# Kernel tuning notes

Hardware: AMD Instinct MI355X
Metric: run time of the kernel (lower is better)

The kernel has to match this reference:

```python
import jax, jax.numpy as jnp
import numpy as np

N_CLUSTERS = 2048
EMBED_DIM = 512
DECAY = 0.99
EPSILON = 1e-05
NORM_EPS = 1e-12  # torch F.normalize default eps


def setup_inputs() -> dict:
    key = jax.random.key(0)
    k1, k2, k3, k4 = jax.random.split(key, 4)
    N = 32768
    return {
        "X": jax.random.normal(k1, (N, EMBED_DIM), dtype=jnp.float32),
        "centroids": jax.random.normal(k2, (N_CLUSTERS, EMBED_DIM), dtype=jnp.float32),
        "ema_cluster_size": jax.random.uniform(k3, (N_CLUSTERS,), dtype=jnp.float32),
        "ema_w": jax.random.normal(k4, (N_CLUSTERS, EMBED_DIM), dtype=jnp.float32),
    }


def reference(X, centroids, ema_cluster_size, ema_w):
    # --- distances on L2-normalized X (F.normalize(X, p=2, dim=1)) ---
    Xn = X / jnp.maximum(jnp.linalg.norm(X, axis=1, keepdims=True), NORM_EPS)
    distances = (
        jnp.sum(Xn * Xn, axis=1, keepdims=True)
        + jnp.sum(centroids * centroids, axis=1)
        - 2.0 * (Xn @ centroids.T)
    )
    cluster_indices = jnp.argmin(distances, axis=1)  # [N]
    onehot = jax.nn.one_hot(cluster_indices, N_CLUSTERS, dtype=X.dtype)  # [N,K]

    # quantized = onehot @ centroids  (gather form, same math)
    quantized = centroids[cluster_indices]  # [N,D]

    # --- EMA codebook update (uses ORIGINAL X, not normalized, per source) ---
    new_size = ema_cluster_size * DECAY + (1.0 - DECAY) * jnp.sum(onehot, axis=0)
    n = jnp.sum(new_size)
    new_size = (new_size + EPSILON) / (n + N_CLUSTERS * EPSILON) * n
    dw = onehot.T @ X  # [K,D] scatter-sum of assigned points
    new_w = ema_w * DECAY + (1.0 - DECAY) * dw
    new_centroids = new_w / new_size[:, None]

    return quantized, cluster_indices[:, None], new_centroids, new_size, new_w
```

## Files before the change

kernel.cpp:

```cpp
#include <hip/hip_runtime.h>
#include <hip/hip_bf16.h>
#include <stdint.h>

#define N_PTS    32768
#define N_CLU    2048
#define DIM      512
#define DECAY    0.99f
#define EPS      1e-5f
#define NORM_EPS 1e-12f
#define MARGIN   0.02f
#define WCAP     24576

#define OUT_Q      0
#define OUT_IDX    (N_PTS*DIM)
#define OUT_NEWC   (OUT_IDX + N_PTS)
#define OUT_SIZE   (OUT_NEWC + N_CLU*DIM)
#define OUT_NEWW   (OUT_SIZE + N_CLU)

typedef _Float16 half8 __attribute__((ext_vector_type(8)));
typedef float f32x4 __attribute__((ext_vector_type(4)));

union H8 { _Float16 h[8]; uint4 u; };

__device__ __forceinline__ unsigned enc_f32(float f) {
    unsigned u = __float_as_uint(f);
    return (u & 0x80000000u) ? ~u : (u | 0x80000000u);
}
__device__ __forceinline__ float dec_f32(unsigned e) {
    unsigned u = (e & 0x80000000u) ? (e & 0x7FFFFFFFu) : ~e;
    return __uint_as_float(u);
}

__global__ void init_kernel(int* __restrict__ counts,
                            int* __restrict__ cursor,
                            int* __restrict__ wl_cnt,
                            float* __restrict__ dw,
                            unsigned long long* __restrict__ best64) {
    int i = blockIdx.x * blockDim.x + threadIdx.x;
    int stride = gridDim.x * blockDim.x;
    if (i == 0) wl_cnt[0] = 0;
    for (int j = i; j < N_CLU; j += stride) { counts[j] = 0; cursor[j] = 0; }
    for (int j = i; j < N_CLU * DIM; j += stride) dw[j] = 0.0f;
    for (int j = i; j < WCAP; j += stride) best64[j] = 0xFFFFFFFFFFFFFFFFULL;
}

__global__ void prep_x_kernel(const float* __restrict__ X,
                              float* __restrict__ rnorm,
                              _Float16* __restrict__ Xh) {
    int row = (blockIdx.x * blockDim.x + threadIdx.x) >> 6;
    int lane = threadIdx.x & 63;
    if (row >= N_PTS) return;
    const float4* xr = (const float4*)(X + (size_t)row * DIM);
    float4 a = xr[2 * lane];
    float4 b = xr[2 * lane + 1];
    float ss = a.x*a.x + a.y*a.y + a.z*a.z + a.w*a.w
             + b.x*b.x + b.y*b.y + b.z*b.z + b.w*b.w;
    #pragma unroll
    for (int off = 32; off > 0; off >>= 1) ss += __shfl_xor(ss, off);
    float rs = 1.0f / fmaxf(sqrtf(ss), NORM_EPS);
    if (lane == 0) rnorm[row] = rs;
    H8 o;
    o.h[0] = (_Float16)(a.x * rs); o.h[1] = (_Float16)(a.y * rs);
    o.h[2] = (_Float16)(a.z * rs); o.h[3] = (_Float16)(a.w * rs);
    o.h[4] = (_Float16)(b.x * rs); o.h[5] = (_Float16)(b.y * rs);
    o.h[6] = (_Float16)(b.z * rs); o.h[7] = (_Float16)(b.w * rs);
    *(uint4*)(Xh + (size_t)row * DIM + lane * 8) = o.u;
}

__global__ void prep_c_kernel(const float* __restrict__ C,
                              float* __restrict__ cnorm2,
                              _Float16* __restrict__ Ch) {
    int row = (blockIdx.x * blockDim.x + threadIdx.x) >> 6;
    int lane = threadIdx.x & 63;
    if (row >= N_CLU) return;
    const float4* cr = (const float4*)(C + (size_t)row * DIM);
    float4 a = cr[2 * lane];
    float4 b = cr[2 * lane + 1];
    float ss = a.x*a.x + a.y*a.y + a.z*a.z + a.w*a.w
             + b.x*b.x + b.y*b.y + b.z*b.z + b.w*b.w;
    #pragma unroll
    for (int off = 32; off > 0; off >>= 1) ss += __shfl_xor(ss, off);
    if (lane == 0) cnorm2[row] = ss;
    H8 o;
    o.h[0] = (_Float16)a.x; o.h[1] = (_Float16)a.y;
    o.h[2] = (_Float16)a.z; o.h[3] = (_Float16)a.w;
    o.h[4] = (_Float16)b.x; o.h[5] = (_Float16)b.y;
    o.h[6] = (_Float16)b.z; o.h[7] = (_Float16)b.w;
    *(uint4*)(Ch + (size_t)row * DIM + lane * 8) = o.u;
}

#define TBM 128
#define TBN 128
#define TBK 32
#define LDS_S 40

__global__ __launch_bounds__(256) void dist_mfma_kernel(
    const _Float16* __restrict__ Xh, const _Float16* __restrict__ Ch,
    const float* __restrict__ cnorm2,
    unsigned long long* __restrict__ tile2) {
    __shared__ _Float16 Ah[TBM * LDS_S];
    __shared__ _Float16 Bh[TBN * LDS_S];

    const int tid = threadIdx.x;
    const int m0 = blockIdx.x * TBM;
    const int n0 = blockIdx.y * TBN;

    const int wid = tid >> 6;
    const int l = tid & 63;
    const int wr = wid >> 1, wc = wid & 1;
    const int lr = l & 15, g = l >> 4;

    const int srow = tid >> 1, shalf = tid & 1;
    const _Float16* srcA = Xh + (size_t)(m0 + srow) * DIM + shalf * 16;
    const _Float16* srcB = Ch + (size_t)(n0 + srow) * DIM + shalf * 16;
    _Float16* dstA = &Ah[srow * LDS_S + shalf * 16];
    _Float16* dstB = &Bh[srow * LDS_S + shalf * 16];

    f32x4 acc[4][4];
    #pragma unroll
    for (int m = 0; m < 4; m++)
        #pragma unroll
        for (int n = 0; n < 4; n++) acc[m][n] = (f32x4){0.f, 0.f, 0.f, 0.f};

    for (int k0 = 0; k0 < DIM; k0 += TBK) {
        const uint4* pa = (const uint4*)(srcA + k0);
        const uint4* pb = (const uint4*)(srcB + k0);
        uint4 a0 = pa[0], a1 = pa[1];
        uint4 b0 = pb[0], b1 = pb[1];
        *(uint4*)dstA = a0; *(uint4*)(dstA + 8) = a1;
        *(uint4*)dstB = b0; *(uint4*)(dstB + 8) = b1;
        __syncthreads();

        half8 af[4], bf[4];
        #pragma unroll
        for (int m = 0; m < 4; m++)
            af[m] = *(const half8*)&Ah[(wr * 64 + m * 16 + lr) * LDS_S + g * 8];
        #pragma unroll
        for (int n = 0; n < 4; n++)
            bf[n] = *(const half8*)&Bh[(wc * 64 + n * 16 + lr) * LDS_S + g * 8];
        #pragma unroll
        for (int m = 0; m < 4; m++)
            #pragma unroll
            for (int n = 0; n < 4; n++)
                acc[m][n] = __builtin_amdgcn_mfma_f32_16x16x32_f16(af[m], bf[n], acc[m][n], 0, 0, 0);
        __syncthreads();
    }

    float cn2[4];
    int coln[4];
    #pragma unroll
    for (int n = 0; n < 4; n++) {
        coln[n] = n0 + wc * 64 + n * 16 + lr;
        cn2[n] = cnorm2[coln[n]];
    }
    const int slot = blockIdx.y * 2 + wc;
    #pragma unroll
    for (int m = 0; m < 4; m++) {
        #pragma unroll
        for (int reg = 0; reg < 4; reg++) {
            unsigned long long b1 = ~0ULL, b2 = ~0ULL;
            #pragma unroll
            for (int n = 0; n < 4; n++) {
                float s = cn2[n] - 2.0f * acc[m][n][reg];
                unsigned long long p =
                    ((unsigned long long)enc_f32(s) << 32) | (unsigned)coln[n];
                if (p < b1) { b2 = b1; b1 = p; }
                else if (p < b2) { b2 = p; }
            }
            #pragma unroll
            for (int off = 1; off < 16; off <<= 1) {
                unsigned long long c1 = __shfl_xor(b1, off);
                unsigned long long c2 = __shfl_xor(b2, off);
                if (c1 < b1) { b2 = (b1 < c2) ? b1 : c2; b1 = c1; }
                else         { b2 = (b2 < c1) ? b2 : c1; }
            }
            if (lr == 0) {
                int R = m0 + wr * 64 + m * 16 + g * 4 + reg;
                size_t o = ((size_t)slot * N_PTS + R) * 2;
                tile2[o] = b1;
                tile2[o + 1] = b2;
            }
        }
    }
}

__global__ void reduce_kernel(const unsigned long long* __restrict__ tile2,
                              int* __restrict__ idxs,
                              int* __restrict__ wl, int* __restrict__ wl_cnt) {
    int i = blockIdx.x * blockDim.x + threadIdx.x;
    if (i >= N_PTS) return;
    unsigned long long b1 = ~0ULL, b2 = ~0ULL;
    #pragma unroll
    for (int j = 0; j < 32; j++) {
        size_t o = ((size_t)j * N_PTS + i) * 2;
        unsigned long long c1 = tile2[o], c2 = tile2[o + 1];
        if (c1 < b1) { b2 = (b1 < c2) ? b1 : c2; b1 = c1; }
        else         { b2 = (b2 < c1) ? b2 : c1; }
    }
    idxs[i] = (int)(unsigned)(b1 & 0xFFFFFFFFu);
    float gap = dec_f32((unsigned)(b2 >> 32)) - dec_f32((unsigned)(b1 >> 32));
    if (gap < MARGIN) {
        int pos = atomicAdd(wl_cnt, 1);
        wl[pos] = i;
    }
}

__global__ void gather_kernel(const float* __restrict__ X,
                              const float* __restrict__ rnorm,
                              const int* __restrict__ wl,
                              const int* __restrict__ wl_cnt,
                              float* __restrict__ Xg) {
    int gw = (blockIdx.x * blockDim.x + threadIdx.x) >> 6;
    int lane = threadIdx.x & 63;
    int n = wl_cnt[0];
    if (n > WCAP) n = WCAP;
    for (int pos = gw; pos < n; pos += 2048) {
        int i = wl[pos];
        float rs = rnorm[i];
        const float4* src = (const float4*)(X + (size_t)i * DIM);
        float4* dst = (float4*)(Xg + (size_t)pos * DIM);
        float4 a = src[2 * lane], b = src[2 * lane + 1];
        a.x *= rs; a.y *= rs; a.z *= rs; a.w *= rs;
        b.x *= rs; b.y *= rs; b.z *= rs; b.w *= rs;
        dst[2 * lane] = a;
        dst[2 * lane + 1] = b;
    }
}

#define BM 128
#define BN 128
#define BK 16

__global__ __launch_bounds__(256) void exact_tile_kernel(
    const float* __restrict__ Xg, const float* __restrict__ C,
    const float* __restrict__ cnorm2, const int* __restrict__ wl_cnt,
    unsigned long long* __restrict__ best64) {
    const int m0 = blockIdx.x * BM;
    int n = wl_cnt[0];
    if (n > WCAP) n = WCAP;
    if (m0 >= n) return;

    __shared__ float As[BK][BM];
    __shared__ float Bs[BK][BN];

    const int tid = threadIdx.x;
    const int tx = tid & 15;
    const int ty = tid >> 4;
    const int n0 = blockIdx.y * BN;

    const int f0 = tid;
    const int f1 = tid + 256;
    const int rowA0 = f0 >> 2, kq0 = f0 & 3;
    const int rowA1 = f1 >> 2, kq1 = f1 & 3;
    const float* Abase0 = Xg + (size_t)(m0 + rowA0) * DIM + kq0 * 4;
    const float* Abase1 = Xg + (size_t)(m0 + rowA1) * DIM + kq1 * 4;
    const float* Bbase0 = C + (size_t)(n0 + rowA0) * DIM + kq0 * 4;
    const float* Bbase1 = C + (size_t)(n0 + rowA1) * DIM + kq1 * 4;

    float acc[8][8];
    #pragma unroll
    for (int r = 0; r < 8; r++)
        #pragma unroll
        for (int c = 0; c < 8; c++) acc[r][c] = 0.0f;

    for (int c0 = 0; c0 < DIM; c0 += BK) {
        float4 va0 = *(const float4*)(Abase0 + c0);
        float4 va1 = *(const float4*)(Abase1 + c0);
        float4 vb0 = *(const float4*)(Bbase0 + c0);
        float4 vb1 = *(const float4*)(Bbase1 + c0);
        As[kq0*4+0][rowA0] = va0.x; As[kq0*4+1][rowA0] = va0.y;
        As[kq0*4+2][rowA0] = va0.z; As[kq0*4+3][rowA0] = va0.w;
        As[kq1*4+0][rowA1] = va1.x; As[kq1*4+1][rowA1] = va1.y;
        As[kq1*4+2][rowA1] = va1.z; As[kq1*4+3][rowA1] = va1.w;
        Bs[kq0*4+0][rowA0] = vb0.x; Bs[kq0*4+1][rowA0] = vb0.y;
        Bs[kq0*4+2][rowA0] = vb0.z; Bs[kq0*4+3][rowA0] = vb0.w;
        Bs[kq1*4+0][rowA1] = vb1.x; Bs[kq1*4+1][rowA1] = vb1.y;
        Bs[kq1*4+2][rowA1] = vb1.z; Bs[kq1*4+3][rowA1] = vb1.w;
        __syncthreads();

        #pragma unroll
        for (int t = 0; t < BK; t++) {
            float4 a0 = *(const float4*)&As[t][ty * 8];
            float4 a1 = *(const float4*)&As[t][ty * 8 + 4];
            float4 b0 = *(const float4*)&Bs[t][tx * 8];
            float4 b1 = *(const float4*)&Bs[t][tx * 8 + 4];
            float a[8] = {a0.x, a0.y, a0.z, a0.w, a1.x, a1.y, a1.z, a1.w};
            float b[8] = {b0.x, b0.y, b0.z, b0.w, b1.x, b1.y, b1.z, b1.w};
            #pragma unroll
            for (int r = 0; r < 8; r++)
                #pragma unroll
                for (int c = 0; c < 8; c++)
                    acc[r][c] = fmaf(a[r], b[c], acc[r][c]);
        }
        __syncthreads();
    }

    #pragma unroll
    for (int r = 0; r < 8; r++) {
        float bs = INFINITY;
        int bi = 0x7FFFFFFF;
        #pragma unroll
        for (int c = 0; c < 8; c++) {
            int gc = n0 + tx * 8 + c;
            float s = cnorm2[gc] - 2.0f * acc[r][c];
            if (s < bs) { bs = s; bi = gc; }
        }
        unsigned long long p =
            ((unsigned long long)enc_f32(bs) << 32) | (unsigned)bi;
        #pragma unroll
        for (int off = 1; off < 16; off <<= 1) {
            unsigned long long q = __shfl_xor(p, off);
            if (q < p) p = q;
        }
        if (tx == 0) atomicMin(best64 + m0 + ty * 8 + r, p);
    }
}

__global__ void writeback_kernel(const unsigned long long* __restrict__ best64,
                                 const int* __restrict__ wl,
                                 const int* __restrict__ wl_cnt,
                                 int* __restrict__ idxs) {
    int pos = blockIdx.x * blockDim.x + threadIdx.x;
    int n = wl_cnt[0];
    if (n > WCAP) n = WCAP;
    if (pos >= n) return;
    idxs[wl[pos]] = (int)(unsigned)(best64[pos] & 0xFFFFFFFFu);
}

__global__ __launch_bounds__(256) void exact_serial_kernel(
    const float* __restrict__ X, const float* __restrict__ C,
    const float* __restrict__ rnorm, const float* __restrict__ cnorm2,
    const int* __restrict__ wl, const int* __restrict__ wl_cnt,
    int* __restrict__ idxs) {
    int gw = (blockIdx.x * blockDim.x + threadIdx.x) >> 6;
    int lane = threadIdx.x & 63;
    int n = wl_cnt[0];
    for (int it = WCAP + gw; it < n; it += 1024) {
        int i = wl[it];
        float rs = rnorm[i];
        const float4* xr = (const float4*)(X + (size_t)i * DIM);
        float4 xa = xr[2 * lane], xb = xr[2 * lane + 1];
        xa.x *= rs; xa.y *= rs; xa.z *= rs; xa.w *= rs;
        xb.x *= rs; xb.y *= rs; xb.z *= rs; xb.w *= rs;
        unsigned long long best = ~0ULL;
        for (int k = 0; k < N_CLU; k++) {
            const float4* cr = (const float4*)(C + (size_t)k * DIM);
            float4 ca = cr[2 * lane], cb = cr[2 * lane + 1];
            float d = xa.x*ca.x + xa.y*ca.y + xa.z*ca.z + xa.w*ca.w
                    + xb.x*cb.x + xb.y*cb.y + xb.z*cb.z + xb.w*cb.w;
            #pragma unroll
            for (int off = 32; off > 0; off >>= 1) d += __shfl_xor(d, off);
            float s = cnorm2[k] - 2.0f * d;
            unsigned long long p =
                ((unsigned long long)enc_f32(s) << 32) | (unsigned)k;
            if (p < best) best = p;
        }
        if (lane == 0) idxs[i] = (int)(unsigned)(best & 0xFFFFFFFFu);
    }
}

__global__ void decode_kernel(const int* __restrict__ idxs,
                              float* __restrict__ out_idx,
                              int* __restrict__ counts) {
    int i = blockIdx.x * blockDim.x + threadIdx.x;
    if (i >= N_PTS) return;
    int lane = threadIdx.x & 63;
    int idx = idxs[i];
    out_idx[i] = (float)idx;
    unsigned long long remaining = __ballot(1);
    while (remaining) {
        int leader = __ffsll((unsigned long long)remaining) - 1;
        int k0 = __shfl(idx, leader);
        unsigned long long mask = __ballot(idx == k0);
        if (lane == leader) atomicAdd(&counts[k0], (int)__popcll(mask));
        remaining &= ~mask;
    }
}

__global__ void quant_kernel(const float* __restrict__ C,
                             const int* __restrict__ idxs,
                             float* __restrict__ outq) {
    int wave = (blockIdx.x * blockDim.x + threadIdx.x) >> 6;
    int lane = threadIdx.x & 63;
    if (wave >= N_PTS) return;
    int idx = idxs[wave];
    const float4* src = (const float4*)(C + (size_t)idx * DIM);
    float4* dst = (float4*)(outq + (size_t)wave * DIM);
    dst[lane] = src[lane];
    dst[lane + 64] = src[lane + 64];
}

__global__ __launch_bounds__(1024) void scan_kernel(const int* __restrict__ counts,
                                                    int* __restrict__ offsets) {
    __shared__ int bufA[N_CLU];
    __shared__ int bufB[N_CLU];
    int t = threadIdx.x;
    bufA[t] = counts[t];
    bufA[t + 1024] = counts[t + 1024];
    __syncthreads();
    int* src = bufA;
    int* dst = bufB;
    for (int d = 1; d < N_CLU; d <<= 1) {
        for (int i = t; i < N_CLU; i += 1024) {
            int v = src[i];
            if (i >= d) v += src[i - d];
            dst[i] = v;
        }
        __syncthreads();
        int* tmp = src; src = dst; dst = tmp;
    }
    for (int i = t; i < N_CLU; i += 1024)
        offsets[i] = (i == 0) ? 0 : src[i - 1];
}

__global__ void place_kernel(const int* __restrict__ idxs,
                             const int* __restrict__ offsets,
                             int* __restrict__ cursor,
                             int* __restrict__ bucket,
                             int* __restrict__ bkey) {
    int i = blockIdx.x * blockDim.x + threadIdx.x;
    if (i >= N_PTS) return;
    int lane = threadIdx.x & 63;
    int k = idxs[i];
    int pos = 0;
    unsigned long long remaining = __ballot(1);
    while (remaining) {
        int leader = __ffsll((unsigned long long)remaining) - 1;
        int k0 = __shfl(k, leader);
        unsigned long long mask = __ballot(k == k0);
        int base = 0;
        if (lane == leader) base = atomicAdd(&cursor[k0], (int)__popcll(mask));
        base = __shfl(base, leader);
        if (k == k0)
            pos = offsets[k0] + base +
                  (int)__popcll(mask & ((1ULL << lane) - 1ULL));
        remaining &= ~mask;
    }
    bucket[pos] = i;
    bkey[pos] = k;
}

__global__ __launch_bounds__(1024) void newsize_kernel(
    const float* __restrict__ ema_size, const int* __restrict__ counts,
    float* __restrict__ out_size) {
    __shared__ float red[16];
    __shared__ float nval;
    int t = threadIdx.x;
    float p0 = ema_size[t] * DECAY + (1.0f - DECAY) * (float)counts[t];
    float p1 = ema_size[t + 1024] * DECAY + (1.0f - DECAY) * (float)counts[t + 1024];
    float s = p0 + p1;
    #pragma unroll
    for (int off = 32; off > 0; off >>= 1) s += __shfl_xor(s, off);
    if ((t & 63) == 0) red[t >> 6] = s;
    __syncthreads();
    if (t == 0) {
        float n = 0.0f;
        for (int i = 0; i < 16; i++) n += red[i];
        nval = n;
    }
    __syncthreads();
    float n = nval;
    float denom = n + (float)N_CLU * EPS;
    out_size[t]        = (p0 + EPS) / denom * n;
    out_size[t + 1024] = (p1 + EPS) / denom * n;
}

#define CHUNK 64
__global__ __launch_bounds__(256) void dw_kernel(
    const float* __restrict__ X, const int* __restrict__ bucket,
    const int* __restrict__ bkey, float* __restrict__ dw) {
    int c0 = blockIdx.x * CHUNK;
    int t = threadIdx.x;
    float accx = 0.0f, accy = 0.0f;
    int prevk = bkey[c0];
    for (int j = 0; j < CHUNK; j++) {
        int pos = c0 + j;
        int k = bkey[pos];
        if (k != prevk) {
            atomicAdd(&dw[(size_t)prevk * DIM + t * 2 + 0], accx);
            atomicAdd(&dw[(size_t)prevk * DIM + t * 2 + 1], accy);
            accx = 0.0f; accy = 0.0f;
            prevk = k;
        }
        int p = bucket[pos];
        float2 v = *(const float2*)(X + (size_t)p * DIM + t * 2);
        accx += v.x; accy += v.y;
    }
    atomicAdd(&dw[(size_t)prevk * DIM + t * 2 + 0], accx);
    atomicAdd(&dw[(size_t)prevk * DIM + t * 2 + 1], accy);
}

__global__ void final_kernel(const float* __restrict__ ema_w,
                             const float* __restrict__ dw,
                             const float* __restrict__ new_size,
                             float* __restrict__ out_neww,
                             float* __restrict__ out_newc) {
    int e = blockIdx.x * blockDim.x + threadIdx.x;
    if (e >= N_CLU * DIM) return;
    int k = e >> 9;
    float nw = ema_w[e] * DECAY + (1.0f - DECAY) * dw[e];
    out_neww[e] = nw;
    out_newc[e] = nw / new_size[k];
}

extern "C" void kernel_launch(void* const* d_in, const int* in_sizes, int n_in,
                              void* d_out, int out_size, void* d_ws, size_t ws_size,
                              hipStream_t stream) {
    const float* X        = (const float*)d_in[0];
    const float* C        = (const float*)d_in[1];
    const float* ema_size = (const float*)d_in[2];
    const float* ema_w    = (const float*)d_in[3];
    float* out = (float*)d_out;

    float* out_q    = out + OUT_Q;
    float* out_idx  = out + OUT_IDX;
    float* out_newc = out + OUT_NEWC;
    float* out_sizep= out + OUT_SIZE;
    float* out_neww = out + OUT_NEWW;

    _Float16* Xh = (_Float16*)out_q;
    unsigned long long* tile2 =
        (unsigned long long*)((char*)out_q + (size_t)N_PTS * DIM * 2);
    float* Xg = (float*)out_q;

    char* ws = (char*)d_ws;
    float* rnorm  = (float*)ws;                                    ws += N_PTS * 4;
    float* cnorm2 = (float*)ws;                                    ws += N_CLU * 4;
    int*   idxs   = (int*)ws;                                      ws += N_PTS * 4;
    int*   counts = (int*)ws;                                      ws += N_CLU * 4;
    int*   offsets= (int*)ws;                                      ws += N_CLU * 4;
    int*   cursor = (int*)ws;                                      ws += N_CLU * 4;
    int*   bucket = (int*)ws;                                      ws += N_PTS * 4;
    int*   bkey   = (int*)ws;                                      ws += N_PTS * 4;
    int*   wl     = (int*)ws;                                      ws += N_PTS * 4;
    int*   wl_cnt = (int*)ws;                                      ws += 16;
    float* dw     = (float*)ws;                                    ws += N_CLU * DIM * 4;
    _Float16* Ch  = (_Float16*)ws;                                 ws += (size_t)N_CLU * DIM * 2;
    unsigned long long* best64 = (unsigned long long*)ws;          ws += (size_t)WCAP * 8;

    init_kernel<<<2048, 256, 0, stream>>>(counts, cursor, wl_cnt, dw, best64);
    prep_x_kernel<<<N_PTS / 4, 256, 0, stream>>>(X, rnorm, Xh);
    prep_c_kernel<<<N_CLU / 4, 256, 0, stream>>>(C, cnorm2, Ch);

    dim3 grid(N_PTS / TBM, N_CLU / TBN);
    dist_mfma_kernel<<<grid, 256, 0, stream>>>(Xh, Ch, cnorm2, tile2);

    reduce_kernel<<<N_PTS / 256, 256, 0, stream>>>(tile2, idxs, wl, wl_cnt);
    gather_kernel<<<512, 256, 0, stream>>>(X, rnorm, wl, wl_cnt, Xg);
    dim3 egrid(WCAP / BM, N_CLU / BN);
    exact_tile_kernel<<<egrid, 256, 0, stream>>>(Xg, C, cnorm2, wl_cnt, best64);
    writeback_kernel<<<WCAP / 256, 256, 0, stream>>>(best64, wl, wl_cnt, idxs);
    exact_serial_kernel<<<256, 256, 0, stream>>>(X, C, rnorm, cnorm2, wl, wl_cnt, idxs);

    decode_kernel<<<N_PTS / 256, 256, 0, stream>>>(idxs, out_idx, counts);
    quant_kernel<<<N_PTS / 4, 256, 0, stream>>>(C, idxs, out_q);
    newsize_kernel<<<1, 1024, 0, stream>>>(ema_size, counts, out_sizep);
    scan_kernel<<<1, 1024, 0, stream>>>(counts, offsets);
    place_kernel<<<N_PTS / 256, 256, 0, stream>>>(idxs, offsets, cursor, bucket, bkey);
    dw_kernel<<<N_PTS / CHUNK, 256, 0, stream>>>(X, bucket, bkey, dw);
    final_kernel<<<(N_CLU * DIM) / 256, 256, 0, stream>>>(ema_w, dw, out_sizep, out_neww, out_newc);
}
```

Measured before the change: 513.7 us.

## Load MFMA tiles directly into LDS and fuse size/scan kernels

The distance GEMM now stages its A and B tiles with global_load_lds (direct global-to-LDS, 16 bytes per lane) instead of loading into registers and storing to LDS. The LDS layout drops the padded row stride, which may raise bank conflicts on the fragment reads. Separately, the new-size EMA kernel and the prefix-scan kernel are merged into one single-block launch to save a kernel launch. The dist kernel's per-iteration structure is otherwise unchanged (no double buffering).

```diff
diff --git a/kernel.cpp b/kernel.cpp
--- a/kernel.cpp
+++ b/kernel.cpp
@@ -29,6 +29,12 @@
 __device__ __forceinline__ float dec_f32(unsigned e) {
     unsigned u = (e & 0x80000000u) ? (e & 0x7FFFFFFFu) : ~e;
     return __uint_as_float(u);
+}
+
+__device__ __forceinline__ void gload_lds16(const void* g, void* l) {
+    __builtin_amdgcn_global_load_lds(
+        (const __attribute__((address_space(1))) uint32_t*)g,
+        (__attribute__((address_space(3))) uint32_t*)l, 16, 0, 0);
 }
 
 __global__ void init_kernel(int* __restrict__ counts,
@@ -92,14 +98,13 @@
 #define TBM 128
 #define TBN 128
 #define TBK 32
-#define LDS_S 40
 
 __global__ __launch_bounds__(256) void dist_mfma_kernel(
     const _Float16* __restrict__ Xh, const _Float16* __restrict__ Ch,
     const float* __restrict__ cnorm2,
     unsigned long long* __restrict__ tile2) {
-    __shared__ _Float16 Ah[TBM * LDS_S];
-    __shared__ _Float16 Bh[TBN * LDS_S];
+    __shared__ _Float16 Ah[TBM * TBK];
+    __shared__ _Float16 Bh[TBN * TBK];
 
     const int tid = threadIdx.x;
     const int m0 = blockIdx.x * TBM;
@@ -110,11 +115,16 @@
     const int wr = wid >> 1, wc = wid & 1;
     const int lr = l & 15, g = l >> 4;
 
-    const int srow = tid >> 1, shalf = tid & 1;
-    const _Float16* srcA = Xh + (size_t)(m0 + srow) * DIM + shalf * 16;
-    const _Float16* srcB = Ch + (size_t)(n0 + srow) * DIM + shalf * 16;
-    _Float16* dstA = &Ah[srow * LDS_S + shalf * 16];
-    _Float16* dstB = &Bh[srow * LDS_S + shalf * 16];
+    const int srow = wid * 16 + (l >> 2);
+    const int skq  = l & 3;
+    const _Float16* srcA0 = Xh + (size_t)(m0 + srow) * DIM + skq * 8;
+    const _Float16* srcA1 = srcA0 + (size_t)64 * DIM;
+    const _Float16* srcB0 = Ch + (size_t)(n0 + srow) * DIM + skq * 8;
+    const _Float16* srcB1 = srcB0 + (size_t)64 * DIM;
+    _Float16* dA0 = Ah + wid * 512;
+    _Float16* dA1 = Ah + 2048 + wid * 512;
+    _Float16* dB0 = Bh + wid * 512;
+    _Float16* dB1 = Bh + 2048 + wid * 512;
 
     f32x4 acc[4][4];
     #pragma unroll
@@ -123,21 +133,19 @@
         for (int n = 0; n < 4; n++) acc[m][n] = (f32x4){0.f, 0.f, 0.f, 0.f};
 
     for (int k0 = 0; k0 < DIM; k0 += TBK) {
-        const uint4* pa = (const uint4*)(srcA + k0);
-        const uint4* pb = (const uint4*)(srcB + k0);
-        uint4 a0 = pa[0], a1 = pa[1];
-        uint4 b0 = pb[0], b1 = pb[1];
-        *(uint4*)dstA = a0; *(uint4*)(dstA + 8) = a1;
-        *(uint4*)dstB = b0; *(uint4*)(dstB + 8) = b1;
+        gload_lds16(srcA0 + k0, dA0);
+        gload_lds16(srcA1 + k0, dA1);
+        gload_lds16(srcB0 + k0, dB0);
+        gload_lds16(srcB1 + k0, dB1);
         __syncthreads();
 
         half8 af[4], bf[4];
         #pragma unroll
         for (int m = 0; m < 4; m++)
-            af[m] = *(const half8*)&Ah[(wr * 64 + m * 16 + lr) * LDS_S + g * 8];
+            af[m] = *(const half8*)&Ah[(wr * 64 + m * 16 + lr) * TBK + g * 8];
         #pragma unroll
         for (int n = 0; n < 4; n++)
-            bf[n] = *(const half8*)&Bh[(wc * 64 + n * 16 + lr) * LDS_S + g * 8];
+            bf[n] = *(const half8*)&Bh[(wc * 64 + n * 16 + lr) * TBK + g * 8];
         #pragma unroll
         for (int m = 0; m < 4; m++)
             #pragma unroll
@@ -390,14 +398,29 @@
     dst[lane + 64] = src[lane + 64];
 }
 
-__global__ __launch_bounds__(1024) void scan_kernel(const int* __restrict__ counts,
-                                                    int* __restrict__ offsets) {
+__global__ __launch_bounds__(1024) void sizescan_kernel(
+    const float* __restrict__ ema_size, const int* __restrict__ counts,
+    float* __restrict__ out_size, int* __restrict__ offsets) {
+    __shared__ float red[16];
+    __shared__ float nval;
     __shared__ int bufA[N_CLU];
     __shared__ int bufB[N_CLU];
     int t = threadIdx.x;
-    bufA[t] = counts[t];
-    bufA[t + 1024] = counts[t + 1024];
+    int c0 = counts[t], c1 = counts[t + 1024];
+    float p0 = ema_size[t] * DECAY + (1.0f - DECAY) * (float)c0;
+    float p1 = ema_size[t + 1024] * DECAY + (1.0f - DECAY) * (float)c1;
+    float s = p0 + p1;
+    #pragma unroll
+    for (int off = 32; off > 0; off >>= 1) s += __shfl_xor(s, off);
+    if ((t & 63) == 0) red[t >> 6] = s;
+    bufA[t] = c0;
+    bufA[t + 1024] = c1;
     __syncthreads();
+    if (t == 0) {
+        float n = 0.0f;
+        for (int i = 0; i < 16; i++) n += red[i];
+        nval = n;
+    }
     int* src = bufA;
     int* dst = bufB;
     for (int d = 1; d < N_CLU; d <<= 1) {
@@ -411,6 +434,10 @@
     }
     for (int i = t; i < N_CLU; i += 1024)
         offsets[i] = (i == 0) ? 0 : src[i - 1];
+    float n = nval;
+    float denom = n + (float)N_CLU * EPS;
+    out_size[t]        = (p0 + EPS) / denom * n;
+    out_size[t + 1024] = (p1 + EPS) / denom * n;
 }
 
 __global__ void place_kernel(const int* __restrict__ idxs,
@@ -438,31 +465,6 @@
     }
     bucket[pos] = i;
     bkey[pos] = k;
-}
-
-__global__ __launch_bounds__(1024) void newsize_kernel(
-    const float* __restrict__ ema_size, const int* __restrict__ counts,
-    float* __restrict__ out_size) {
-    __shared__ float red[16];
-    __shared__ float nval;
-    int t = threadIdx.x;
-    float p0 = ema_size[t] * DECAY + (1.0f - DECAY) * (float)counts[t];
-    float p1 = ema_size[t + 1024] * DECAY + (1.0f - DECAY) * (float)counts[t + 1024];
-    float s = p0 + p1;
-    #pragma unroll
-    for (int off = 32; off > 0; off >>= 1) s += __shfl_xor(s, off);
-    if ((t & 63) == 0) red[t >> 6] = s;
-    __syncthreads();
-    if (t == 0) {
-        float n = 0.0f;
-        for (int i = 0; i < 16; i++) n += red[i];
-        nval = n;
-    }
-    __syncthreads();
-    float n = nval;
-    float denom = n + (float)N_CLU * EPS;
-    out_size[t]        = (p0 + EPS) / denom * n;
-    out_size[t + 1024] = (p1 + EPS) / denom * n;
 }
 
 #define CHUNK 64
@@ -554,8 +556,7 @@
 
     decode_kernel<<<N_PTS / 256, 256, 0, stream>>>(idxs, out_idx, counts);
     quant_kernel<<<N_PTS / 4, 256, 0, stream>>>(C, idxs, out_q);
-    newsize_kernel<<<1, 1024, 0, stream>>>(ema_size, counts, out_sizep);
-    scan_kernel<<<1, 1024, 0, stream>>>(counts, offsets);
+    sizescan_kernel<<<1, 1024, 0, stream>>>(ema_size, counts, out_sizep, offsets);
     place_kernel<<<N_PTS / 256, 256, 0, stream>>>(idxs, offsets, cursor, bucket, bkey);
     dw_kernel<<<N_PTS / CHUNK, 256, 0, stream>>>(X, bucket, bkey, dw);
     final_kernel<<<(N_CLU * DIM) / 256, 256, 0, stream>>>(ema_w, dw, out_sizep, out_neww, out_newc);
```

Result: faster. 489.0 us (-4.8%).
